# Performance work log

Measured on AMD Instinct MI355X. Metric: run time of the kernel, lower is better.

Reference implementation:

```python
import jax, jax.numpy as jnp
import numpy as np

N, E, IN = 50000, 800000, 128   # nodes, edges, input feature dim
H, C = 8, 32                    # heads, per-head channels
HC = H * C                      # 256 = concat width
NEG_SLOPE = 0.2
BN_EPS = 1e-5


def _gat_conv(x, src, dst, W, a_src, a_dst, b, heads, out_ch, concat):
    """PyG-style GATConv (eval mode, self-loops already in src/dst)."""
    n = x.shape[0]
    h = (x @ W).reshape(n, heads, out_ch)                 # [N,H,C]
    alpha_s = (h * a_src).sum(-1)                         # [N,H]
    alpha_d = (h * a_dst).sum(-1)                         # [N,H]
    e = jax.nn.leaky_relu(alpha_s[src] + alpha_d[dst], NEG_SLOPE)  # [Etot,H]
    # segment softmax over destination nodes (every node has a self-loop)
    emax = jax.ops.segment_max(e, dst, num_segments=n)    # [N,H]
    e = jnp.exp(e - emax[dst])
    denom = jax.ops.segment_sum(e, dst, num_segments=n)
    alpha = e / (denom[dst] + 1e-16)                      # [Etot,H]
    msg = h[src] * alpha[:, :, None]                      # [Etot,H,C]
    out = jax.ops.segment_sum(msg, dst, num_segments=n)   # [N,H,C]
    out = out.reshape(n, heads * out_ch) if concat else out.mean(axis=1)
    return out + b


def _bn(y, g, beta, m, v):
    return (y - m) * jax.lax.rsqrt(v + BN_EPS) * g + beta


def setup_inputs() -> dict:
    key = jax.random.key(0)
    ks = jax.random.split(key, 32)
    def p(i, shape, s=0.1):
        return jax.random.normal(ks[i], shape, dtype=jnp.float32) * s
    x = jax.random.normal(ks[0], (N, IN), dtype=jnp.float32)
    edge_index = jax.random.randint(ks[1], (2, E), 0, N, dtype=jnp.int32)
    d = dict(
        x=x, edge_index=edge_index,
        W1=p(2, (IN, HC)), a_src1=p(3, (H, C)), a_dst1=p(4, (H, C)), b1=p(5, (HC,)),
        bn1_g=jnp.ones((HC,), jnp.float32), bn1_b=jnp.zeros((HC,), jnp.float32),
        bn1_m=p(6, (HC,)), bn1_v=jax.random.uniform(ks[7], (HC,), jnp.float32, 0.5, 1.5),
        W2=p(8, (HC, HC)), a_src2=p(9, (H, C)), a_dst2=p(10, (H, C)), b2=p(11, (HC,)),
        bn2_g=jnp.ones((HC,), jnp.float32), bn2_b=jnp.zeros((HC,), jnp.float32),
        bn2_m=p(12, (HC,)), bn2_v=jax.random.uniform(ks[13], (HC,), jnp.float32, 0.5, 1.5),
        W3=p(14, (HC, C)), a_src3=p(15, (1, C)), a_dst3=p(16, (1, C)), b3=p(17, (C,)),
        Ws1=p(18, (IN, HC)), bs1=p(19, (HC,)),
        Ws2=p(20, (HC, C)), bs2=p(21, (C,)),
    )
    return d


def reference(x, edge_index, W1, a_src1, a_dst1, b1, bn1_g, bn1_b, bn1_m, bn1_v,
              W2, a_src2, a_dst2, b2, bn2_g, bn2_b, bn2_m, bn2_v,
              W3, a_src3, a_dst3, b3, Ws1, bs1, Ws2, bs2):
    n = x.shape[0]
    loops = jnp.arange(n, dtype=edge_index.dtype)
    src = jnp.concatenate([edge_index[0], loops])   # PyG add_self_loops=True
    dst = jnp.concatenate([edge_index[1], loops])
    x0 = x @ Ws1 + bs1                               # skip1
    h = _gat_conv(x, src, dst, W1, a_src1, a_dst1, b1, H, C, True)
    h = jax.nn.elu(_bn(h, bn1_g, bn1_b, bn1_m, bn1_v)) + x0
    xs = h @ Ws2 + bs2                               # skip2
    h2 = _gat_conv(h, src, dst, W2, a_src2, a_dst2, b2, H, C, True)
    h2 = jax.nn.elu(_bn(h2, bn2_g, bn2_b, bn2_m, bn2_v))
    out = _gat_conv(h2, src, dst, W3, a_src3, a_dst3, b3, 1, C, False) + xs
    return out
```

## Files before the change

kernel.cpp:

```cpp
#include <hip/hip_runtime.h>
#include <hip/hip_bf16.h>

#define NEG_SLOPE 0.2f
#define BN_EPS 1e-5f
#define BSH 8
#define STASH_CAP 6400

typedef __attribute__((ext_vector_type(8))) short bf16x8;
typedef __attribute__((ext_vector_type(4))) float f32x4;

#if defined(__has_builtin)
#if __has_builtin(__builtin_amdgcn_cvt_f32_fp8) && __has_builtin(__builtin_amdgcn_cvt_pk_fp8_f32)
#define HW_FP8 1
#endif
#endif

__device__ __forceinline__ float bf2f(unsigned short u) {
    union { unsigned int i; float f; } x;
    x.i = ((unsigned int)u) << 16;
    return x.f;
}
__device__ __forceinline__ unsigned short f2bf(float f) {
    __hip_bfloat16 b = __float2bfloat16(f);
    return *reinterpret_cast<unsigned short*>(&b);
}
__device__ __forceinline__ float lrelu(float v) {
    return v > 0.f ? v : NEG_SLOPE * v;
}
__device__ __forceinline__ void gload_lds16(const void* g, void* l) {
    __builtin_amdgcn_global_load_lds(
        (const __attribute__((address_space(1))) unsigned int*)(g),
        (__attribute__((address_space(3))) unsigned int*)(l),
        16, 0, 0);
}

__device__ __forceinline__ unsigned char f8enc(float f) {
#ifdef HW_FP8
    int p = __builtin_amdgcn_cvt_pk_fp8_f32(f, 0.f, 0, false);
    return (unsigned char)(p & 0xff);
#else
    float a = fabsf(f);
    unsigned int sign = (__float_as_uint(f) >> 31) << 7;
    if (a < 0.0009765625f) return (unsigned char)sign;
    a = fminf(a, 448.f);
    unsigned int bits = __float_as_uint(a);
    int e = (int)((bits >> 23) & 0xff) - 127;
    unsigned int mant = bits & 0x7fffff;
    if (e < -6) {
        int q = (int)(a * 512.f + 0.5f);
        if (q >= 8) return (unsigned char)(sign | 0x08);
        return (unsigned char)(sign | q);
    }
    unsigned int m = mant >> 20;
    unsigned int rem = mant & 0xfffff;
    if (rem > 0x80000 || (rem == 0x80000 && (m & 1))) m++;
    if (m == 8) { m = 0; e++; }
    if (e > 8) { e = 8; m = 6; }
    return (unsigned char)(sign | ((unsigned int)(e + 7) << 3) | m);
#endif
}
template <int SEL>
__device__ __forceinline__ float f8dec(unsigned int w) {
#ifdef HW_FP8
    return __builtin_amdgcn_cvt_f32_fp8(w, SEL);
#else
    unsigned int b = (w >> (SEL * 8)) & 0xff;
    unsigned int s = b >> 7, em = b & 0x7f;
    float mag;
    if (em >= 8) {
        unsigned int bits = (((em >> 3) + 120) << 23) | ((em & 7) << 20);
        mag = __uint_as_float(bits);
    } else {
        mag = (float)em * 0.001953125f;
    }
    return s ? -mag : mag;
#endif
}

__device__ __forceinline__ int block_scan_incl(int v, int t) {
    int lane = t & 63, w = t >> 6;
    int sv = v;
    #pragma unroll
    for (int off = 1; off < 64; off <<= 1) {
        int u = __shfl_up(sv, off);
        if (lane >= off) sv += u;
    }
    __shared__ int ws_[4];
    if (lane == 63) ws_[w] = sv;
    __syncthreads();
    if (t == 0) {
        int a = 0;
        #pragma unroll
        for (int k = 0; k < 4; k++) { int x = ws_[k]; ws_[k] = a; a += x; }
    }
    __syncthreads();
    return sv + ws_[w];
}

__global__ __launch_bounds__(256) void bucket_count(const int* __restrict__ dstl,
                                                    int E, int N, int NB,
                                                    int* __restrict__ gHist) {
    __shared__ int h[256];
    int t = threadIdx.x;
    h[t] = 0;
    __syncthreads();
    int Etot = E + N;
    for (int i = blockIdx.x * 256 + t; i < Etot; i += gridDim.x * 256) {
        int d = (i < E) ? dstl[i] : (i - E);
        atomicAdd(&h[d >> BSH], 1);
    }
    __syncthreads();
    if (t < NB && h[t]) atomicAdd(&gHist[t], h[t]);
}

__global__ __launch_bounds__(256) void bucket_scan(const int* __restrict__ gHist,
                                                   int* __restrict__ bases,
                                                   int* __restrict__ gCursor, int NB) {
    int t = threadIdx.x;
    int v = (t < NB) ? gHist[t] : 0;
    int incl = block_scan_incl(v, t);
    if (t < NB) { bases[t] = incl - v; gCursor[t] = incl - v; }
}

__global__ __launch_bounds__(256) void bucket_scatter(const int* __restrict__ srcl,
                                                      const int* __restrict__ dstl,
                                                      int E, int N, int NB,
                                                      int* __restrict__ gCursor,
                                                      unsigned int* __restrict__ bktEdges) {
    __shared__ unsigned int stage[4096];
    __shared__ int hist[256];
    __shared__ int bexcl[257];
    __shared__ int curk[256];
    __shared__ int gbase[256];
    int t = threadIdx.x;
    int Etot = E + N;
    int begin = blockIdx.x * 4096;

    hist[t] = 0;
    __syncthreads();

    unsigned int ent[16];
    int eb[16];
    #pragma unroll
    for (int k = 0; k < 16; k++) {
        int i = begin + k * 256 + t;
        if (i < Etot) {
            int s, d;
            if (i < E) { s = srcl[i]; d = dstl[i]; }
            else       { s = d = i - E; }
            eb[k] = d >> BSH;
            ent[k] = ((unsigned int)s << BSH) | (unsigned int)(d & 255);
            atomicAdd(&hist[eb[k]], 1);
        } else eb[k] = -1;
    }
    __syncthreads();

    int v = hist[t];
    int incl = block_scan_incl(v, t);
    bexcl[t] = incl - v;
    curk[t] = incl - v;
    if (t == 255) bexcl[256] = incl;
    __syncthreads();

    #pragma unroll
    for (int k = 0; k < 16; k++) {
        if (eb[k] >= 0) {
            int slot = atomicAdd(&curk[eb[k]], 1);
            stage[slot] = ent[k];
        }
    }
    if (t < NB) {
        int cnt = hist[t];
        gbase[t] = cnt ? atomicAdd(&gCursor[t], cnt) : 0;
    }
    __syncthreads();

    int total = bexcl[256];
    for (int p = t; p < total; p += 256) {
        int lo = 0, hi = NB - 1;
        while (lo < hi) {
            int mid = (lo + hi + 1) >> 1;
            if (bexcl[mid] <= p) lo = mid; else hi = mid - 1;
        }
        bktEdges[gbase[lo] + (p - bexcl[lo])] = stage[p];
    }
}

__global__ __launch_bounds__(256) void bucket_to_csr(const unsigned int* __restrict__ bktEdges,
                                                     const int* __restrict__ bases,
                                                     const int* __restrict__ gCursor,
                                                     int* __restrict__ indptr,
                                                     int* __restrict__ esrc,
                                                     int N, int NB, int Etot) {
    __shared__ int nh[256];
    __shared__ int ncur[256];
    __shared__ unsigned int stash[STASH_CAP];
    int b = blockIdx.x, t = threadIdx.x;
    int base = bases[b];
    int cnt = gCursor[b] - base;
    int nodeBase = b << BSH;

    nh[t] = 0;
    __syncthreads();
    for (int p = t; p < cnt; p += 256) {
        unsigned int e = bktEdges[base + p];
        if (p < STASH_CAP) stash[p] = e;
        atomicAdd(&nh[e & 255], 1);
    }
    __syncthreads();
    int v = nh[t];
    int incl = block_scan_incl(v, t);
    int excl = incl - v;
    ncur[t] = excl;
    if (nodeBase + t < N) indptr[nodeBase + t] = base + excl;
    __syncthreads();
    for (int p = t; p < cnt; p += 256) {
        unsigned int e = (p < STASH_CAP) ? stash[p] : bktEdges[base + p];
        int slot = atomicAdd(&ncur[e & 255], 1);
        esrc[base + slot] = (int)(e >> BSH);
    }
    if (b == 0 && t == 0) indptr[N] = Etot;
}

__global__ __launch_bounds__(256) void prep_all(const float* __restrict__ x,
                                                unsigned short* __restrict__ xb, int n4x,
                                                const float* __restrict__ W1,
                                                const float* __restrict__ Ws1,
                                                const float* __restrict__ W2,
                                                const float* __restrict__ Ws2,
                                                const float* __restrict__ W3,
                                                unsigned short* __restrict__ Wcat1,
                                                unsigned short* __restrict__ Wcat2,
                                                unsigned short* __restrict__ W3t) {
    int i = blockIdx.x * 256 + threadIdx.x;
    if (i < n4x) {
        float4 v = reinterpret_cast<const float4*>(x)[i];
        ushort4 o;
        o.x = f2bf(v.x); o.y = f2bf(v.y); o.z = f2bf(v.z); o.w = f2bf(v.w);
        reinterpret_cast<ushort4*>(xb)[i] = o;
        return;
    }
    int j = i - n4x;
    if (j < 32768) {
        int m = j >> 7, k = j & 127;
        Wcat1[j] = f2bf(W1[k * 256 + m]);
    } else if (j < 65536) {
        int q = j - 32768; int m = q >> 7, k = q & 127;
        Wcat1[32768 + q] = f2bf(Ws1[k * 256 + m]);
    } else if (j < 131072) {
        int q = j - 65536; int m = q >> 8, k = q & 255;
        Wcat2[q] = f2bf(W2[k * 256 + m]);
    } else if (j < 139264) {
        int q = j - 131072; int m = q >> 8, k = q & 255;
        Wcat2[65536 + q] = f2bf(Ws2[k * 32 + m]);
    } else if (j < 147456) {
        int q = j - 139264; int m = q >> 8, k = q & 255;
        W3t[q] = f2bf(W3[k * 32 + m]);
    }
}

__global__ __launch_bounds__(256) void gemm_tile(const unsigned short* __restrict__ A,
                                                 const unsigned short* __restrict__ Bt,
                                                 unsigned short* __restrict__ outBf,
                                                 unsigned char* __restrict__ outQ,
                                                 unsigned short* __restrict__ outSk,
                                                 const float* __restrict__ biasSk,
                                                 int M, int K, int NCtot, int split,
                                                 int ldBf, int ldSk) {
    __shared__ __align__(16) char smem[2][2][8192];
    int t = threadIdx.x;
    int w = t >> 6, lane = t & 63;
    int l16 = lane & 15, quad = lane >> 4;
    int warp_r = w >> 1, warp_c = w & 1;
    int rowBase = blockIdx.y * 128;
    int colBase = blockIdx.x * 128;

    int row_l = t & 127;
    int jchunk = t >> 7;
    int arow_st = rowBase + row_l; if (arow_st >= M) arow_st = M - 1;
    int bcol_st = colBase + row_l; if (bcol_st >= NCtot) bcol_st = NCtot - 1;
    const unsigned short* aRow = A + (size_t)arow_st * K;
    const unsigned short* bRow = Bt + (size_t)bcol_st * K;

    f32x4 acc[4][4];
    #pragma unroll
    for (int i = 0; i < 4; i++)
        #pragma unroll
        for (int j = 0; j < 4; j++) acc[i][j] = (f32x4){0.f, 0.f, 0.f, 0.f};

    auto stage = [&](int buf, int k0) {
        #pragma unroll
        for (int j = 0; j < 2; j++) {
            int chunk = j * 2 + jchunk;
            gload_lds16(aRow + k0 + chunk * 8, &smem[buf][0][(size_t)j * 4096 + (size_t)t * 16]);
            gload_lds16(bRow + k0 + chunk * 8, &smem[buf][1][(size_t)j * 4096 + (size_t)t * 16]);
        }
    };

    stage(0, 0);
    __syncthreads();
    int niter = K >> 5;
    for (int it = 0; it < niter; ++it) {
        if (it + 1 < niter) stage((it + 1) & 1, (it + 1) << 5);
        const char* Ab = &smem[it & 1][0][0];
        const char* Bb = &smem[it & 1][1][0];
        bf16x8 a[4], b[4];
        #pragma unroll
        for (int i = 0; i < 4; i++)
            a[i] = *reinterpret_cast<const bf16x8*>(Ab + quad * 2048 + (warp_r * 64 + i * 16 + l16) * 16);
        #pragma unroll
        for (int j = 0; j < 4; j++)
            b[j] = *reinterpret_cast<const bf16x8*>(Bb + quad * 2048 + (warp_c * 64 + j * 16 + l16) * 16);
        #pragma unroll
        for (int i = 0; i < 4; i++)
            #pragma unroll
            for (int j = 0; j < 4; j++)
                acc[i][j] = __builtin_amdgcn_mfma_f32_16x16x32_bf16(a[i], b[j], acc[i][j], 0, 0, 0);
        __syncthreads();
    }

    #pragma unroll
    for (int i = 0; i < 4; i++) {
        #pragma unroll
        for (int r = 0; r < 4; r++) {
            int row = rowBase + warp_r * 64 + i * 16 + quad * 4 + r;
            if (row >= M) continue;
            #pragma unroll
            for (int j = 0; j < 4; j++) {
                int c = colBase + warp_c * 64 + j * 16 + l16;
                if (c >= NCtot) continue;
                float v = acc[i][j][r];
                if (c < split) {
                    outBf[(size_t)row * ldBf + c] = f2bf(v);
                    if (outQ) outQ[(size_t)row * ldBf + c] = f8enc(v);
                } else {
                    outSk[(size_t)row * ldSk + (c - split)] = f2bf(v + biasSk[c - split]);
                }
            }
        }
    }
}

__global__ __launch_bounds__(256) void alpha256(const unsigned short* __restrict__ h,
                                                const float* __restrict__ a_s,
                                                const float* __restrict__ a_d,
                                                float* __restrict__ as_out,
                                                float* __restrict__ ad_out, int N) {
    int t = threadIdx.x;
    int n = blockIdx.x * 4 + (t >> 6);
    if (n >= N) return;
    int lane = t & 63, lane4 = lane * 4;
    ushort4 hv = *reinterpret_cast<const ushort4*>(&h[(size_t)n * 256 + lane4]);
    float4 sv = *reinterpret_cast<const float4*>(&a_s[lane4]);
    float4 dv = *reinterpret_cast<const float4*>(&a_d[lane4]);
    float h0 = bf2f(hv.x), h1 = bf2f(hv.y), h2 = bf2f(hv.z), h3 = bf2f(hv.w);
    float va = h0 * sv.x + h1 * sv.y + h2 * sv.z + h3 * sv.w;
    float vd = h0 * dv.x + h1 * dv.y + h2 * dv.z + h3 * dv.w;
    #pragma unroll
    for (int off = 1; off < 8; off <<= 1) {
        va += __shfl_xor(va, off);
        vd += __shfl_xor(vd, off);
    }
    if ((lane & 7) == 0) {
        as_out[n * 8 + (lane >> 3)] = va;
        ad_out[n * 8 + (lane >> 3)] = vd;
    }
}

__global__ __launch_bounds__(256) void alpha32(const unsigned short* __restrict__ h,
                                               const float* __restrict__ a_s,
                                               const float* __restrict__ a_d,
                                               float* __restrict__ as_out,
                                               float* __restrict__ ad_out, int N) {
    int t = threadIdx.x;
    int lane = t & 63;
    int n = blockIdx.x * 32 + (t >> 6) * 8 + (lane >> 3);
    int c4 = (lane & 7) * 4;
    if (n >= N) return;
    ushort4 hv = *reinterpret_cast<const ushort4*>(&h[(size_t)n * 32 + c4]);
    float4 sv = *reinterpret_cast<const float4*>(&a_s[c4]);
    float4 dv = *reinterpret_cast<const float4*>(&a_d[c4]);
    float h0 = bf2f(hv.x), h1 = bf2f(hv.y), h2 = bf2f(hv.z), h3 = bf2f(hv.w);
    float va = h0 * sv.x + h1 * sv.y + h2 * sv.z + h3 * sv.w;
    float vd = h0 * dv.x + h1 * dv.y + h2 * dv.z + h3 * dv.w;
    #pragma unroll
    for (int off = 1; off < 8; off <<= 1) {
        va += __shfl_xor(va, off);
        vd += __shfl_xor(vd, off);
    }
    if ((lane & 7) == 0) {
        as_out[n] = va;
        ad_out[n] = vd;
    }
}

template <int MODE>
__global__ __launch_bounds__(256) void agg256(const unsigned char* __restrict__ hq,
                                              const float* __restrict__ as,
                                              const float* __restrict__ ad,
                                              const int* __restrict__ indptr,
                                              const int* __restrict__ esrc,
                                              const float* __restrict__ bias,
                                              const float* __restrict__ bn_g,
                                              const float* __restrict__ bn_b,
                                              const float* __restrict__ bn_m,
                                              const float* __restrict__ bn_v,
                                              const unsigned short* __restrict__ skip,
                                              unsigned short* __restrict__ out, int N) {
    int t = threadIdx.x;
    int n = blockIdx.x * 4 + (t >> 6);
    if (n >= N) return;
    int lane = t & 63;
    int e_sub = lane >> 3, h_sub = lane & 7;
    int ch_head = lane >> 3;
    int lane4 = lane * 4;
    int start = indptr[n], end = indptr[n + 1];
    int cnt = end - start;

    float adh = ad[n * 8 + h_sub];

    float4 acc = make_float4(0.f, 0.f, 0.f, 0.f);
    float sm = 0.f;
    int nfull = cnt & ~7;
    int i0 = start;
    int s_l = 0; float w8 = 0.f;
    if (nfull) {
        s_l = esrc[i0 + e_sub];
        w8 = __expf(lrelu(as[s_l * 8 + h_sub] + adh));
    }
    while (i0 < start + nfull) {
        int s_cur = s_l;
        float w_cur = w8;
        i0 += 8;
        if (i0 < start + nfull) {
            s_l = esrc[i0 + e_sub];
            w8 = __expf(lrelu(as[s_l * 8 + h_sub] + adh));
        }
        sm += w_cur;
        unsigned int hv[8];
        #pragma unroll
        for (int e = 0; e < 8; e++) {
            int se = __shfl(s_cur, e * 8);
            hv[e] = *reinterpret_cast<const unsigned int*>(&hq[(size_t)se * 256 + lane4]);
        }
        #pragma unroll
        for (int e = 0; e < 8; e++) {
            float we = __shfl(w_cur, e * 8 + ch_head);
            acc.x = fmaf(we, f8dec<0>(hv[e]), acc.x);
            acc.y = fmaf(we, f8dec<1>(hv[e]), acc.y);
            acc.z = fmaf(we, f8dec<2>(hv[e]), acc.z);
            acc.w = fmaf(we, f8dec<3>(hv[e]), acc.w);
        }
    }
    int rem = cnt - nfull;
    if (rem) {
        int idx = i0 + e_sub;
        int s_r = esrc[idx < end ? idx : end - 1];
        float w_r = (idx < end) ? __expf(lrelu(as[s_r * 8 + h_sub] + adh)) : 0.f;
        sm += w_r;
        #pragma unroll
        for (int e = 0; e < 8; e++) {
            if (e < rem) {
                int se = __shfl(s_r, e * 8);
                float we = __shfl(w_r, e * 8 + ch_head);
                unsigned int hv = *reinterpret_cast<const unsigned int*>(&hq[(size_t)se * 256 + lane4]);
                acc.x = fmaf(we, f8dec<0>(hv), acc.x);
                acc.y = fmaf(we, f8dec<1>(hv), acc.y);
                acc.z = fmaf(we, f8dec<2>(hv), acc.z);
                acc.w = fmaf(we, f8dec<3>(hv), acc.w);
            }
        }
    }
    #pragma unroll
    for (int off = 8; off < 64; off <<= 1) sm += __shfl_xor(sm, off);
    float il = 1.f / (sm + 1e-16f);
    float il_c = __shfl(il, ch_head);

    float4 bv  = *reinterpret_cast<const float4*>(&bias[lane4]);
    float4 gv  = *reinterpret_cast<const float4*>(&bn_g[lane4]);
    float4 bbv = *reinterpret_cast<const float4*>(&bn_b[lane4]);
    float4 mv  = *reinterpret_cast<const float4*>(&bn_m[lane4]);
    float4 vv  = *reinterpret_cast<const float4*>(&bn_v[lane4]);
    float o[4] = {acc.x * il_c + bv.x, acc.y * il_c + bv.y,
                  acc.z * il_c + bv.z, acc.w * il_c + bv.w};
    float g[4] = {gv.x, gv.y, gv.z, gv.w}, bb[4] = {bbv.x, bbv.y, bbv.z, bbv.w};
    float m[4] = {mv.x, mv.y, mv.z, mv.w}, vr[4] = {vv.x, vv.y, vv.z, vv.w};
    float sk[4] = {0.f, 0.f, 0.f, 0.f};
    if (MODE == 1) {
        ushort4 s4 = *reinterpret_cast<const ushort4*>(&skip[(size_t)n * 256 + lane4]);
        sk[0] = bf2f(s4.x); sk[1] = bf2f(s4.y); sk[2] = bf2f(s4.z); sk[3] = bf2f(s4.w);
    }
    ushort4 res;
    unsigned short* rp = &res.x;
    #pragma unroll
    for (int j = 0; j < 4; j++) {
        float val = (o[j] - m[j]) * rsqrtf(vr[j] + BN_EPS) * g[j] + bb[j];
        val = val > 0.f ? val : (__expf(val) - 1.f);
        val += sk[j];
        rp[j] = f2bf(val);
    }
    *reinterpret_cast<ushort4*>(&out[(size_t)n * 256 + lane4]) = res;
}

__global__ __launch_bounds__(256) void agg32(const unsigned short* __restrict__ h3,
                                             const float* __restrict__ as,
                                             const float* __restrict__ ad,
                                             const int* __restrict__ indptr,
                                             const int* __restrict__ esrc,
                                             const float* __restrict__ b3,
                                             const unsigned short* __restrict__ xs,
                                             float* __restrict__ out, int N) {
    int t = threadIdx.x;
    int n = blockIdx.x * 4 + (t >> 6);
    if (n >= N) return;
    int lane = t & 63;
    int e_sub = lane >> 3, c4 = (lane & 7) * 4;
    int start = indptr[n], end = indptr[n + 1];
    float adn = ad[n];

    float4 acc = make_float4(0.f, 0.f, 0.f, 0.f);
    float sm = 0.f;
    int i0 = start;
    for (; i0 + 16 <= end; i0 += 16) {
        int sA = esrc[i0 + e_sub];
        int sB = esrc[i0 + 8 + e_sub];
        float wA = __expf(lrelu(as[sA] + adn));
        float wB = __expf(lrelu(as[sB] + adn));
        sm += wA + wB;
        ushort4 hA = *reinterpret_cast<const ushort4*>(&h3[(size_t)sA * 32 + c4]);
        ushort4 hB = *reinterpret_cast<const ushort4*>(&h3[(size_t)sB * 32 + c4]);
        acc.x = fmaf(wA, bf2f(hA.x), acc.x); acc.y = fmaf(wA, bf2f(hA.y), acc.y);
        acc.z = fmaf(wA, bf2f(hA.z), acc.z); acc.w = fmaf(wA, bf2f(hA.w), acc.w);
        acc.x = fmaf(wB, bf2f(hB.x), acc.x); acc.y = fmaf(wB, bf2f(hB.y), acc.y);
        acc.z = fmaf(wB, bf2f(hB.z), acc.z); acc.w = fmaf(wB, bf2f(hB.w), acc.w);
    }
    for (; i0 < end; i0 += 8) {
        int idx = i0 + e_sub;
        bool valid = idx < end;
        if (valid) {
            int s = esrc[idx];
            float w = __expf(lrelu(as[s] + adn));
            sm += w;
            ushort4 hv = *reinterpret_cast<const ushort4*>(&h3[(size_t)s * 32 + c4]);
            acc.x = fmaf(w, bf2f(hv.x), acc.x);
            acc.y = fmaf(w, bf2f(hv.y), acc.y);
            acc.z = fmaf(w, bf2f(hv.z), acc.z);
            acc.w = fmaf(w, bf2f(hv.w), acc.w);
        }
    }
    #pragma unroll
    for (int off = 8; off < 64; off <<= 1) {
        sm    += __shfl_xor(sm, off);
        acc.x += __shfl_xor(acc.x, off);
        acc.y += __shfl_xor(acc.y, off);
        acc.z += __shfl_xor(acc.z, off);
        acc.w += __shfl_xor(acc.w, off);
    }
    if (e_sub == 0) {
        float il = 1.f / (sm + 1e-16f);
        float4 bv = *reinterpret_cast<const float4*>(&b3[c4]);
        ushort4 xv = *reinterpret_cast<const ushort4*>(&xs[(size_t)n * 32 + c4]);
        float4 o;
        o.x = acc.x * il + bv.x + bf2f(xv.x);
        o.y = acc.y * il + bv.y + bf2f(xv.y);
        o.z = acc.z * il + bv.z + bf2f(xv.z);
        o.w = acc.w * il + bv.w + bf2f(xv.w);
        *reinterpret_cast<float4*>(&out[(size_t)n * 32 + c4]) = o;
    }
}

extern "C" void kernel_launch(void* const* d_in, const int* in_sizes, int n_in,
                              void* d_out, int out_size, void* d_ws, size_t ws_size,
                              hipStream_t stream) {
    const float* x      = (const float*)d_in[0];
    const int*   eidx   = (const int*)  d_in[1];
    const float* W1     = (const float*)d_in[2];
    const float* a_src1 = (const float*)d_in[3];
    const float* a_dst1 = (const float*)d_in[4];
    const float* b1     = (const float*)d_in[5];
    const float* bn1_g  = (const float*)d_in[6];
    const float* bn1_b  = (const float*)d_in[7];
    const float* bn1_m  = (const float*)d_in[8];
    const float* bn1_v  = (const float*)d_in[9];
    const float* W2     = (const float*)d_in[10];
    const float* a_src2 = (const float*)d_in[11];
    const float* a_dst2 = (const float*)d_in[12];
    const float* b2     = (const float*)d_in[13];
    const float* bn2_g  = (const float*)d_in[14];
    const float* bn2_b  = (const float*)d_in[15];
    const float* bn2_m  = (const float*)d_in[16];
    const float* bn2_v  = (const float*)d_in[17];
    const float* W3     = (const float*)d_in[18];
    const float* a_src3 = (const float*)d_in[19];
    const float* a_dst3 = (const float*)d_in[20];
    const float* b3     = (const float*)d_in[21];
    const float* Ws1    = (const float*)d_in[22];
    const float* bs1    = (const float*)d_in[23];
    const float* Ws2    = (const float*)d_in[24];
    const float* bs2    = (const float*)d_in[25];

    const int N = in_sizes[0] / 128;
    const int E = in_sizes[1] / 2;
    const int Etot = E + N;
    const int NB = (N + 255) >> 8;
    const int* srcl = eidx;
    const int* dstl = eidx + E;

    char* ws = (char*)d_ws;
    size_t off = 0;
    auto alloc = [&](size_t bytes) -> void* {
        void* p = ws + off;
        off += (bytes + 255) & ~(size_t)255;
        return p;
    };
    unsigned short* xb    = (unsigned short*)alloc((size_t)N * 128 * 2);
    unsigned short* feat  = (unsigned short*)alloc((size_t)N * 256 * 2);
    unsigned short* hbuf  = (unsigned short*)alloc((size_t)N * 256 * 2);
    unsigned char*  hq    = (unsigned char*)alloc((size_t)N * 256);
    unsigned short* h2b   = (unsigned short*)alloc((size_t)N * 256 * 2);
    unsigned short* featb = (unsigned short*)alloc((size_t)N * 256 * 2);
    unsigned short* xsbuf = (unsigned short*)alloc((size_t)N * 32 * 2);
    unsigned short* h3b   = (unsigned short*)alloc((size_t)N * 32 * 2);
    float*          asb   = (float*)alloc((size_t)N * 8 * 4);
    float*          adb   = (float*)alloc((size_t)N * 8 * 4);
    unsigned short* Wcat1 = (unsigned short*)alloc((size_t)512 * 128 * 2);
    unsigned short* Wcat2 = (unsigned short*)alloc((size_t)288 * 256 * 2);
    unsigned short* W3t   = (unsigned short*)alloc((size_t)32 * 256 * 2);
    int* gHist   = (int*)alloc((size_t)NB * 4);
    int* bases   = (int*)alloc((size_t)NB * 4);
    int* gCursor = (int*)alloc((size_t)NB * 4);
    unsigned int* bktEdges = (unsigned int*)alloc((size_t)Etot * 4);
    int* indptr  = (int*)alloc((size_t)(N + 1) * 4);
    int* esrc    = (int*)alloc((size_t)Etot * 4);
    (void)ws_size; (void)n_in; (void)out_size;

    hipMemsetAsync(gHist, 0, (size_t)NB * 4, stream);
    bucket_count<<<256, 256, 0, stream>>>(dstl, E, N, NB, gHist);
    bucket_scan<<<1, 256, 0, stream>>>(gHist, bases, gCursor, NB);
    bucket_scatter<<<(Etot + 4095) / 4096, 256, 0, stream>>>(srcl, dstl, E, N, NB,
                                                             gCursor, bktEdges);
    bucket_to_csr<<<NB, 256, 0, stream>>>(bktEdges, bases, gCursor, indptr, esrc,
                                          N, NB, Etot);

    int n4x = N * 128 / 4;
    prep_all<<<(n4x + 147456 + 255) / 256, 256, 0, stream>>>(x, xb, n4x,
                                                             W1, Ws1, W2, Ws2, W3,
                                                             Wcat1, Wcat2, W3t);

    int gy128 = (N + 127) / 128;
    int gn4 = (N + 3) / 4;

    gemm_tile<<<dim3(4, gy128), 256, 0, stream>>>(xb, Wcat1, hbuf, hq, feat, bs1,
                                                  N, 128, 512, 256, 256, 256);
    alpha256<<<gn4, 256, 0, stream>>>(hbuf, a_src1, a_dst1, asb, adb, N);
    agg256<1><<<gn4, 256, 0, stream>>>(hq, asb, adb, indptr, esrc, b1,
                                       bn1_g, bn1_b, bn1_m, bn1_v, feat, h2b, N);

    gemm_tile<<<dim3(3, gy128), 256, 0, stream>>>(h2b, Wcat2, hbuf, hq, xsbuf, bs2,
                                                  N, 256, 288, 256, 256, 32);
    alpha256<<<gn4, 256, 0, stream>>>(hbuf, a_src2, a_dst2, asb, adb, N);
    agg256<0><<<gn4, 256, 0, stream>>>(hq, asb, adb, indptr, esrc, b2,
                                       bn2_g, bn2_b, bn2_m, bn2_v, nullptr, featb, N);

    gemm_tile<<<dim3(1, gy128), 256, 0, stream>>>(featb, W3t, h3b, nullptr, h3b, nullptr,
                                                  N, 256, 32, 32, 32, 32);
    alpha32<<<(N + 31) / 32, 256, 0, stream>>>(h3b, a_src3, a_dst3, asb, adb, N);
    agg32<<<gn4, 256, 0, stream>>>(h3b, asb, adb, indptr, esrc, b3, xsbuf,
                                   (float*)d_out, N);
}
```

Before: 411.1 us.

## Fuse attention logit computation into GEMM epilogue and use packed FP8 decode

```diff
diff --git a/kernel.cpp b/kernel.cpp
--- a/kernel.cpp
+++ b/kernel.cpp
@@ -8,10 +8,14 @@
 
 typedef __attribute__((ext_vector_type(8))) short bf16x8;
 typedef __attribute__((ext_vector_type(4))) float f32x4;
+typedef __attribute__((ext_vector_type(2))) float f32x2;
 
 #if defined(__has_builtin)
 #if __has_builtin(__builtin_amdgcn_cvt_f32_fp8) && __has_builtin(__builtin_amdgcn_cvt_pk_fp8_f32)
 #define HW_FP8 1
+#endif
+#if __has_builtin(__builtin_amdgcn_cvt_pk_f32_fp8)
+#define HW_FP8_PK 1
 #endif
 #endif
 
@@ -74,6 +78,21 @@
         mag = (float)em * 0.001953125f;
     }
     return s ? -mag : mag;
+#endif
+}
+__device__ __forceinline__ void fma_f8x4(float we, unsigned int wv, float4& acc) {
+#ifdef HW_FP8_PK
+    f32x2 lo = __builtin_amdgcn_cvt_pk_f32_fp8((int)wv, false);
+    f32x2 hi = __builtin_amdgcn_cvt_pk_f32_fp8((int)wv, true);
+    acc.x = fmaf(we, lo[0], acc.x);
+    acc.y = fmaf(we, lo[1], acc.y);
+    acc.z = fmaf(we, hi[0], acc.z);
+    acc.w = fmaf(we, hi[1], acc.w);
+#else
+    acc.x = fmaf(we, f8dec<0>(wv), acc.x);
+    acc.y = fmaf(we, f8dec<1>(wv), acc.y);
+    acc.z = fmaf(we, f8dec<2>(wv), acc.z);
+    acc.w = fmaf(we, f8dec<3>(wv), acc.w);
 #endif
 }
 
@@ -265,6 +284,10 @@
                                                  unsigned char* __restrict__ outQ,
                                                  unsigned short* __restrict__ outSk,
                                                  const float* __restrict__ biasSk,
+                                                 const float* __restrict__ aS,
+                                                 const float* __restrict__ aD,
+                                                 float* __restrict__ asOut,
+                                                 float* __restrict__ adOut,
                                                  int M, int K, int NCtot, int split,
                                                  int ldBf, int ldSk) {
     __shared__ __align__(16) char smem[2][2][8192];
@@ -319,6 +342,39 @@
         __syncthreads();
     }
 
+    if (aS && colBase < split) {
+        int c0 = colBase + warp_c * 64 + l16;
+        int hbase = (colBase + warp_c * 64) >> 5;
+        float as0 = aS[c0],      ad0 = aD[c0];
+        float as1 = aS[c0 + 16], ad1 = aD[c0 + 16];
+        float as2 = aS[c0 + 32], ad2 = aD[c0 + 32];
+        float as3 = aS[c0 + 48], ad3 = aD[c0 + 48];
+        #pragma unroll
+        for (int i = 0; i < 4; i++) {
+            #pragma unroll
+            for (int r = 0; r < 4; r++) {
+                float va0 = acc[i][0][r] * as0 + acc[i][1][r] * as1;
+                float vd0 = acc[i][0][r] * ad0 + acc[i][1][r] * ad1;
+                float va1 = acc[i][2][r] * as2 + acc[i][3][r] * as3;
+                float vd1 = acc[i][2][r] * ad2 + acc[i][3][r] * ad3;
+                #pragma unroll
+                for (int off = 1; off < 16; off <<= 1) {
+                    va0 += __shfl_xor(va0, off);
+                    vd0 += __shfl_xor(vd0, off);
+                    va1 += __shfl_xor(va1, off);
+                    vd1 += __shfl_xor(vd1, off);
+                }
+                int row = rowBase + warp_r * 64 + i * 16 + quad * 4 + r;
+                if (l16 == 0 && row < M) {
+                    asOut[row * 8 + hbase]     = va0;
+                    adOut[row * 8 + hbase]     = vd0;
+                    asOut[row * 8 + hbase + 1] = va1;
+                    adOut[row * 8 + hbase + 1] = vd1;
+                }
+            }
+        }
+    }
+
     #pragma unroll
     for (int i = 0; i < 4; i++) {
         #pragma unroll
@@ -331,39 +387,13 @@
                 if (c >= NCtot) continue;
                 float v = acc[i][j][r];
                 if (c < split) {
-                    outBf[(size_t)row * ldBf + c] = f2bf(v);
-                    if (outQ) outQ[(size_t)row * ldBf + c] = f8enc(v);
+                    if (outBf) outBf[(size_t)row * ldBf + c] = f2bf(v);
+                    if (outQ)  outQ[(size_t)row * ldBf + c] = f8enc(v);
                 } else {
                     outSk[(size_t)row * ldSk + (c - split)] = f2bf(v + biasSk[c - split]);
                 }
             }
         }
-    }
-}
-
-__global__ __launch_bounds__(256) void alpha256(const unsigned short* __restrict__ h,
-                                                const float* __restrict__ a_s,
-                                                const float* __restrict__ a_d,
-                                                float* __restrict__ as_out,
-                                                float* __restrict__ ad_out, int N) {
-    int t = threadIdx.x;
-    int n = blockIdx.x * 4 + (t >> 6);
-    if (n >= N) return;
-    int lane = t & 63, lane4 = lane * 4;
-    ushort4 hv = *reinterpret_cast<const ushort4*>(&h[(size_t)n * 256 + lane4]);
-    float4 sv = *reinterpret_cast<const float4*>(&a_s[lane4]);
-    float4 dv = *reinterpret_cast<const float4*>(&a_d[lane4]);
-    float h0 = bf2f(hv.x), h1 = bf2f(hv.y), h2 = bf2f(hv.z), h3 = bf2f(hv.w);
-    float va = h0 * sv.x + h1 * sv.y + h2 * sv.z + h3 * sv.w;
-    float vd = h0 * dv.x + h1 * dv.y + h2 * dv.z + h3 * dv.w;
-    #pragma unroll
-    for (int off = 1; off < 8; off <<= 1) {
-        va += __shfl_xor(va, off);
-        vd += __shfl_xor(vd, off);
-    }
-    if ((lane & 7) == 0) {
-        as_out[n * 8 + (lane >> 3)] = va;
-        ad_out[n * 8 + (lane >> 3)] = vd;
     }
 }
 
@@ -446,10 +476,7 @@
         #pragma unroll
         for (int e = 0; e < 8; e++) {
             float we = __shfl(w_cur, e * 8 + ch_head);
-            acc.x = fmaf(we, f8dec<0>(hv[e]), acc.x);
-            acc.y = fmaf(we, f8dec<1>(hv[e]), acc.y);
-            acc.z = fmaf(we, f8dec<2>(hv[e]), acc.z);
-            acc.w = fmaf(we, f8dec<3>(hv[e]), acc.w);
+            fma_f8x4(we, hv[e], acc);
         }
     }
     int rem = cnt - nfull;
@@ -464,10 +491,7 @@
                 int se = __shfl(s_r, e * 8);
                 float we = __shfl(w_r, e * 8 + ch_head);
                 unsigned int hv = *reinterpret_cast<const unsigned int*>(&hq[(size_t)se * 256 + lane4]);
-                acc.x = fmaf(we, f8dec<0>(hv), acc.x);
-                acc.y = fmaf(we, f8dec<1>(hv), acc.y);
-                acc.z = fmaf(we, f8dec<2>(hv), acc.z);
-                acc.w = fmaf(we, f8dec<3>(hv), acc.w);
+                fma_f8x4(we, hv, acc);
             }
         }
     }
@@ -615,7 +639,6 @@
     };
     unsigned short* xb    = (unsigned short*)alloc((size_t)N * 128 * 2);
     unsigned short* feat  = (unsigned short*)alloc((size_t)N * 256 * 2);
-    unsigned short* hbuf  = (unsigned short*)alloc((size_t)N * 256 * 2);
     unsigned char*  hq    = (unsigned char*)alloc((size_t)N * 256);
     unsigned short* h2b   = (unsigned short*)alloc((size_t)N * 256 * 2);
     unsigned short* featb = (unsigned short*)alloc((size_t)N * 256 * 2);
@@ -650,19 +673,20 @@
     int gy128 = (N + 127) / 128;
     int gn4 = (N + 3) / 4;
 
-    gemm_tile<<<dim3(4, gy128), 256, 0, stream>>>(xb, Wcat1, hbuf, hq, feat, bs1,
+    gemm_tile<<<dim3(4, gy128), 256, 0, stream>>>(xb, Wcat1, nullptr, hq, feat, bs1,
+                                                  a_src1, a_dst1, asb, adb,
                                                   N, 128, 512, 256, 256, 256);
-    alpha256<<<gn4, 256, 0, stream>>>(hbuf, a_src1, a_dst1, asb, adb, N);
     agg256<1><<<gn4, 256, 0, stream>>>(hq, asb, adb, indptr, esrc, b1,
                                        bn1_g, bn1_b, bn1_m, bn1_v, feat, h2b, N);
 
-    gemm_tile<<<dim3(3, gy128), 256, 0, stream>>>(h2b, Wcat2, hbuf, hq, xsbuf, bs2,
+    gemm_tile<<<dim3(3, gy128), 256, 0, stream>>>(h2b, Wcat2, nullptr, hq, xsbuf, bs2,
+                                                  a_src2, a_dst2, asb, adb,
                                                   N, 256, 288, 256, 256, 32);
-    alpha256<<<gn4, 256, 0, stream>>>(hbuf, a_src2, a_dst2, asb, adb, N);
     agg256<0><<<gn4, 256, 0, stream>>>(hq, asb, adb, indptr, esrc, b2,
                                        bn2_g, bn2_b, bn2_m, bn2_v, nullptr, featb, N);
 
     gemm_tile<<<dim3(1, gy128), 256, 0, stream>>>(featb, W3t, h3b, nullptr, h3b, nullptr,
+                                                  nullptr, nullptr, nullptr, nullptr,
                                                   N, 256, 32, 32, 32, 32);
     alpha32<<<(N + 31) / 32, 256, 0, stream>>>(h3b, a_src3, a_dst3, asb, adb, N);
     agg32<<<gn4, 256, 0, stream>>>(h3b, asb, adb, indptr, esrc, b3, xsbuf,
```

Result: no change. 404.5 us (-1.6%).
